# Performance work log

Measured on AMD Instinct MI355X. Metric: run time of the kernel, lower is better.

## Reference

```python
import jax, jax.numpy as jnp
import numpy as np

N = 100000
E = 1000000
N_FEAT = 128
N_HID = 16
N_HEAD = 8
HIDDEN = N_HID * N_HEAD  # 128
N_CLASS = 64
NEG_SLOPE = 0.2


def layer_norm(x, g, b, eps=1e-5):
    mu = x.mean(-1, keepdims=True)
    var = ((x - mu) ** 2).mean(-1, keepdims=True)
    return (x - mu) * jax.lax.rsqrt(var + eps) * g + b


def gat_conv(x, src, dst, W, a_src, a_dst, bias, concat):
    # Standard GATConv math (PyG): project, per-head additive attention,
    # softmax over incoming edges (self-loops included), weighted scatter-sum.
    H, C = a_src.shape
    n = x.shape[0]
    h = (x @ W).reshape(n, H, C)                      # [N,H,C]
    al = jnp.einsum('nhc,hc->nh', h, a_src)           # [N,H]
    ar = jnp.einsum('nhc,hc->nh', h, a_dst)
    e = jax.nn.leaky_relu(al[src] + ar[dst], NEG_SLOPE)  # [E',H]
    m = jax.ops.segment_max(e, dst, num_segments=n)
    m = jnp.where(jnp.isfinite(m), m, 0.0)
    ee = jnp.exp(e - m[dst])
    den = jax.ops.segment_sum(ee, dst, num_segments=n)
    alpha = ee / (den[dst] + 1e-16)                   # [E',H]
    out = jax.ops.segment_sum(h[src] * alpha[:, :, None], dst, num_segments=n)
    out = out.reshape(n, H * C) if concat else out.mean(1)
    return out + bias, h, alpha


def setup_inputs() -> dict:
    key = jax.random.key(0)
    ks = jax.random.split(key, 20)
    s = lambda *sh: 1.0 / np.sqrt(sh[-1])
    inp = {
        'x': jax.random.normal(ks[0], (N, N_FEAT), jnp.float32),
        'edge_index': jax.random.randint(ks[1], (2, E), 0, N, jnp.int32),
        # layer 1: n_feat -> n_hid x n_head (concat)
        'W1': jax.random.normal(ks[2], (N_FEAT, HIDDEN), jnp.float32) * s(N_FEAT),
        'a_src1': jax.random.normal(ks[3], (N_HEAD, N_HID), jnp.float32) * s(N_HID),
        'a_dst1': jax.random.normal(ks[4], (N_HEAD, N_HID), jnp.float32) * s(N_HID),
        'b1': jnp.zeros((HIDDEN,), jnp.float32),
        'g1': jnp.ones((HIDDEN,), jnp.float32),
        'be1': jnp.zeros((HIDDEN,), jnp.float32),
        # layer 2: hidden -> hidden (concat)
        'W2': jax.random.normal(ks[5], (HIDDEN, HIDDEN), jnp.float32) * s(HIDDEN),
        'a_src2': jax.random.normal(ks[6], (N_HEAD, N_HID), jnp.float32) * s(N_HID),
        'a_dst2': jax.random.normal(ks[7], (N_HEAD, N_HID), jnp.float32) * s(N_HID),
        'b2': jnp.zeros((HIDDEN,), jnp.float32),
        'g2': jnp.ones((HIDDEN,), jnp.float32),
        'be2': jnp.zeros((HIDDEN,), jnp.float32),
        # out layer: hidden -> n_class, 1 head, concat=False
        'W3': jax.random.normal(ks[8], (HIDDEN, N_CLASS), jnp.float32) * s(HIDDEN),
        'a_src3': jax.random.normal(ks[9], (1, N_CLASS), jnp.float32) * s(N_CLASS),
        'a_dst3': jax.random.normal(ks[10], (1, N_CLASS), jnp.float32) * s(N_CLASS),
        'b3': jnp.zeros((N_CLASS,), jnp.float32),
        'g3': jnp.ones((N_CLASS,), jnp.float32),
        'be3': jnp.zeros((N_CLASS,), jnp.float32),
    }
    return inp


def reference(x, edge_index, W1, a_src1, a_dst1, b1, g1, be1,
              W2, a_src2, a_dst2, b2, g2, be2,
              W3, a_src3, a_dst3, b3, g3, be3):
    # add self loops (GATConv default)
    loops = jnp.arange(N, dtype=edge_index.dtype)
    src = jnp.concatenate([edge_index[0], loops])
    dst = jnp.concatenate([edge_index[1], loops])
    # Transductive path, eval mode (dropout is identity)
    x, _, _ = gat_conv(x, src, dst, W1, a_src1, a_dst1, b1, concat=True)
    x = jax.nn.elu(layer_norm(x, g1, be1))
    x, _, _ = gat_conv(x, src, dst, W2, a_src2, a_dst2, b2, concat=True)
    x = jax.nn.elu(layer_norm(x, g2, be2))
    x, _, _ = gat_conv(x, src, dst, W3, a_src3, a_dst3, b3, concat=False)
    x = layer_norm(x, g3, be3)
    return x
```

## Files before the change

kernel.cpp:

```cpp
#include <hip/hip_runtime.h>
#include <math.h>

#define N_NODES 100000
#define N_EDGES 1000000
#define EP_EDGES (N_EDGES + N_NODES)
#define NBKT ((N_NODES + 255) / 256)

typedef short bf16x8 __attribute__((ext_vector_type(8)));
typedef float f32x4 __attribute__((ext_vector_type(4)));


__device__ inline unsigned bf16pack(float a, float b) {
    unsigned ua = __float_as_uint(a);
    unsigned ub = __float_as_uint(b);
    ua += 0x7FFFu + ((ua >> 16) & 1u);
    ub += 0x7FFFu + ((ub >> 16) & 1u);
    return (ua >> 16) | (ub & 0xFFFF0000u);
}

__device__ inline unsigned short bf16r(float a) {
    unsigned u = __float_as_uint(a);
    u += 0x7FFFu + ((u >> 16) & 1u);
    return (unsigned short)(u >> 16);
}

__device__ inline int swz(int o) { return o ^ (((o >> 8) & 7) << 4); }


__global__ void bkt_count(const int* __restrict__ ei, int* __restrict__ bktCnt) {
    __shared__ int hist[NBKT];
    int tid = threadIdx.x;
    for (int j = tid; j < NBKT; j += 256) hist[j] = 0;
    __syncthreads();
    int e0 = blockIdx.x * 4096;
    int e1 = min(e0 + 4096, EP_EDGES);
    for (int e = e0 + tid; e < e1; e += 256) {
        int d = (e < N_EDGES) ? ei[N_EDGES + e] : (e - N_EDGES);
        atomicAdd(&hist[d >> 8], 1);
    }
    __syncthreads();
    for (int j = tid; j < NBKT; j += 256) {
        int c = hist[j];
        if (c) atomicAdd(&bktCnt[j], c);
    }
}

__global__ void bkt_scan(const int* __restrict__ bktCnt, int* __restrict__ bktBase,
                         int* __restrict__ bktCursor, int* __restrict__ rs) {
    __shared__ int tmp[512];
    int tid = threadIdx.x;
    int v = (tid < NBKT) ? bktCnt[tid] : 0;
    tmp[tid] = v;
    __syncthreads();
    int run = v;
    for (int off = 1; off < 512; off <<= 1) {
        int add = (tid >= off) ? tmp[tid - off] : 0;
        __syncthreads();
        run += add;
        tmp[tid] = run;
        __syncthreads();
    }
    if (tid <= NBKT) {
        int base = run - v;
        bktBase[tid] = base;
        if (tid < NBKT) bktCursor[tid] = base;
    }
    if (tid == 0) rs[N_NODES] = EP_EDGES;
}

__global__ void bkt_scatter(const int* __restrict__ ei, int* __restrict__ bktCursor,
                            unsigned* __restrict__ bktEdges) {
    __shared__ int hist[NBKT], chunk[NBKT];
    int tid = threadIdx.x;
    for (int j = tid; j < NBKT; j += 256) hist[j] = 0;
    __syncthreads();
    int e0 = blockIdx.x * 2048;
    int e1 = min(e0 + 2048, EP_EDGES);
    for (int e = e0 + tid; e < e1; e += 256) {
        int d = (e < N_EDGES) ? ei[N_EDGES + e] : (e - N_EDGES);
        atomicAdd(&hist[d >> 8], 1);
    }
    __syncthreads();
    for (int j = tid; j < NBKT; j += 256) {
        int c = hist[j];
        chunk[j] = c ? atomicAdd(&bktCursor[j], c) : 0;
        hist[j] = 0;
    }
    __syncthreads();
    for (int e = e0 + tid; e < e1; e += 256) {
        int s, d;
        if (e < N_EDGES) { s = ei[e]; d = ei[N_EDGES + e]; }
        else             { s = d = e - N_EDGES; }
        int b = d >> 8;
        int off = atomicAdd(&hist[b], 1);
        bktEdges[chunk[b] + off] = (unsigned)s | ((unsigned)(d & 255) << 24);
    }
}

__global__ void bkt_final(const unsigned* __restrict__ bktEdges, const int* __restrict__ bktBase,
                          int* __restrict__ rs, int* __restrict__ csr_src) {
    __shared__ int hist[256], excl[256], tmp[256], cur[256];
    int tid = threadIdx.x;
    int b = blockIdx.x;
    int base = bktBase[b], end = bktBase[b + 1];
    hist[tid] = 0;
    __syncthreads();
    for (int i = base + tid; i < end; i += 256)
        atomicAdd(&hist[bktEdges[i] >> 24], 1);
    __syncthreads();
    int v = hist[tid];
    tmp[tid] = v;
    __syncthreads();
    int run = v;
    for (int off = 1; off < 256; off <<= 1) {
        int add = (tid >= off) ? tmp[tid - off] : 0;
        __syncthreads();
        run += add;
        tmp[tid] = run;
        __syncthreads();
    }
    excl[tid] = run - v;
    cur[tid] = 0;
    int node = b * 256 + tid;
    if (node < N_NODES) rs[node] = base + excl[tid];
    __syncthreads();
    for (int i = base + tid; i < end; i += 256) {
        unsigned u = bktEdges[i];
        int d = u >> 24;
        int pos = base + excl[d] + atomicAdd(&cur[d], 1);
        csr_src[pos] = (int)(u & 0xFFFFFFu);
    }
}


template <int COUT>
__global__ void wt_prep(const float* __restrict__ W, unsigned short* __restrict__ Wt) {
    int t = blockIdx.x * 256 + threadIdx.x;
    if (t >= 128 * COUT) return;
    int k = t / COUT, c = t % COUT;
    Wt[c * 128 + k] = bf16r(W[t]);
}


template <int COUT, int H, bool IN_F32>
__launch_bounds__(256)
__global__ void gemm_mfma(const void* __restrict__ Xv, const unsigned short* __restrict__ Wt,
                          const float* __restrict__ a_src, const float* __restrict__ a_dst,
                          unsigned* __restrict__ hb16, float* __restrict__ al,
                          float* __restrict__ ar, int n) {
    constexpr int NT = COUT / 16;
    __shared__ unsigned char lds[16384 + COUT * 256 + 1024];
    unsigned char* sx = lds;
    unsigned char* sw = lds + 16384;
    float* sc = (float*)sw;

    int tid = threadIdx.x;
    int row0 = blockIdx.x * 64;
    int lane = tid & 63;
    int wv = tid >> 6;

    if (IN_F32) {
        const float* Xf = (const float*)Xv;
        for (int c = tid; c < 1024; c += 256) {
            int o = c * 16;
            int row = o >> 8;
            int k0 = (o & 255) >> 1;
            int gr = row0 + row;
            float4 f0 = make_float4(0.f, 0.f, 0.f, 0.f), f1 = f0;
            if (gr < n) {
                f0 = *(const float4*)(Xf + (size_t)gr * 128 + k0);
                f1 = *(const float4*)(Xf + (size_t)gr * 128 + k0 + 4);
            }
            *(uint4*)(sx + swz(o)) = make_uint4(bf16pack(f0.x, f0.y), bf16pack(f0.z, f0.w),
                                                bf16pack(f1.x, f1.y), bf16pack(f1.z, f1.w));
        }
    } else {
        const unsigned char* Xb = (const unsigned char*)Xv;
        for (int c = tid; c < 1024; c += 256) {
            int o = c * 16;
            int row = o >> 8;
            int gr = row0 + row;
            uint4 v = make_uint4(0u, 0u, 0u, 0u);
            if (gr < n) v = *(const uint4*)(Xb + (size_t)gr * 256 + (o & 255));
            *(uint4*)(sx + swz(o)) = v;
        }
    }
    for (int c = tid; c < COUT * 16; c += 256) {
        int o = c * 16;
        *(uint4*)(sw + swz(o)) = *(const uint4*)((const unsigned char*)Wt + o);
    }
    __syncthreads();

    f32x4 acc[NT];
#pragma unroll
    for (int t = 0; t < NT; ++t) acc[t] = (f32x4){0.f, 0.f, 0.f, 0.f};
    int arow = wv * 16 + (lane & 15);
    int kg = lane >> 4;
#pragma unroll
    for (int s = 0; s < 4; ++s) {
        int ko = s * 64 + kg * 16;
        bf16x8 a = *(const bf16x8*)(sx + swz(arow * 256 + ko));
#pragma unroll
        for (int t = 0; t < NT; ++t) {
            bf16x8 bfr = *(const bf16x8*)(sw + swz((t * 16 + (lane & 15)) * 256 + ko));
            acc[t] = __builtin_amdgcn_mfma_f32_16x16x32_bf16(a, bfr, acc[t], 0, 0, 0);
        }
    }
    __syncthreads();

#pragma unroll
    for (int t = 0; t < NT; ++t)
#pragma unroll
        for (int i = 0; i < 4; ++i)
            sc[(wv * 16 + kg * 4 + i) * (COUT + 4) + t * 16 + (lane & 15)] = acc[t][i];
    __syncthreads();

    constexpr int NCG = COUT / 8;
    constexpr int ROWS = 64 * NCG / 256;
    int tc = tid % NCG, tr = tid / NCG;
    float asv[8], adv[8];
#pragma unroll
    for (int j = 0; j < 8; ++j) {
        asv[j] = a_src[tc * 8 + j];
        adv[j] = a_dst[tc * 8 + j];
    }
#pragma unroll
    for (int i = 0; i < ROWS; ++i) {
        int row = tr * ROWS + i;
        int gr = row0 + row;
        float h8[8];
        *(float4*)&h8[0] = *(const float4*)(sc + row * (COUT + 4) + tc * 8);
        *(float4*)&h8[4] = *(const float4*)(sc + row * (COUT + 4) + tc * 8 + 4);
        float pa = 0.f, pb = 0.f;
#pragma unroll
        for (int j = 0; j < 8; ++j) {
            pa = fmaf(h8[j], asv[j], pa);
            pb = fmaf(h8[j], adv[j], pb);
        }
        if (COUT / H == 16) {
            pa += __shfl_xor(pa, 1);
            pb += __shfl_xor(pb, 1);
            if ((tc & 1) == 0 && gr < n) {
                al[gr * H + (tc >> 1)] = pa;
                ar[gr * H + (tc >> 1)] = pb;
            }
        } else {
            pa += __shfl_xor(pa, 1); pb += __shfl_xor(pb, 1);
            pa += __shfl_xor(pa, 2); pb += __shfl_xor(pb, 2);
            pa += __shfl_xor(pa, 4); pb += __shfl_xor(pb, 4);
            if (tc == 0 && gr < n) {
                al[gr] = pa;
                ar[gr] = pb;
            }
        }
        if (gr < n) {
            *(uint4*)(hb16 + (size_t)gr * (COUT / 2) + tc * 4) =
                make_uint4(bf16pack(h8[0], h8[1]), bf16pack(h8[2], h8[3]),
                           bf16pack(h8[4], h8[5]), bf16pack(h8[6], h8[7]));
        }
    }
}


template <int H, int COUT, bool DO_ELU, bool OUTBF>
__launch_bounds__(256)
__global__ void gat_fused(const unsigned* __restrict__ hb16, const float* __restrict__ al,
                          const float* __restrict__ ar, const int* __restrict__ row_start,
                          const int* __restrict__ csr_src, const float* __restrict__ bias,
                          const float* __restrict__ gamma, const float* __restrict__ beta,
                          void* __restrict__ outx, int n) {
    constexpr bool PAIR = (COUT == 128);
    constexpr int C = COUT / H;
    int node = blockIdx.x * 4 + (threadIdx.x >> 6);
    node = __builtin_amdgcn_readfirstlane(node);
    int l = threadIdx.x & 63;
    if (node >= n) return;

    int c0 = PAIR ? 2 * l : l;
    int hc = c0 / C;
    float arh = ar[node * H + hc];

    int rsv = row_start[node];
    int deg = row_start[node + 1] - rsv;
    const int* sp = csr_src + rsv;
    const unsigned short* hbs = (const unsigned short*)hb16;

    float acc0 = 0.f, acc1 = 0.f, den = 0.f;

    int k = 0;
    for (; k + 4 <= deg; k += 4) {
        int s0 = sp[k + 0], s1 = sp[k + 1], s2 = sp[k + 2], s3 = sp[k + 3];
        float a0 = al[s0 * H + hc], a1 = al[s1 * H + hc];
        float a2 = al[s2 * H + hc], a3 = al[s3 * H + hc];
        float e0 = a0 + arh; e0 = (e0 >= 0.f) ? e0 : 0.2f * e0;
        float e1 = a1 + arh; e1 = (e1 >= 0.f) ? e1 : 0.2f * e1;
        float e2 = a2 + arh; e2 = (e2 >= 0.f) ? e2 : 0.2f * e2;
        float e3 = a3 + arh; e3 = (e3 >= 0.f) ? e3 : 0.2f * e3;
        float w0 = __expf(e0), w1 = __expf(e1), w2 = __expf(e2), w3 = __expf(e3);
        den += (w0 + w1) + (w2 + w3);
        if (PAIR) {
            unsigned u0 = hb16[(size_t)s0 * 64 + l];
            unsigned u1 = hb16[(size_t)s1 * 64 + l];
            unsigned u2 = hb16[(size_t)s2 * 64 + l];
            unsigned u3 = hb16[(size_t)s3 * 64 + l];
            acc0 = fmaf(w0, __uint_as_float(u0 << 16), acc0);
            acc1 = fmaf(w0, __uint_as_float(u0 & 0xFFFF0000u), acc1);
            acc0 = fmaf(w1, __uint_as_float(u1 << 16), acc0);
            acc1 = fmaf(w1, __uint_as_float(u1 & 0xFFFF0000u), acc1);
            acc0 = fmaf(w2, __uint_as_float(u2 << 16), acc0);
            acc1 = fmaf(w2, __uint_as_float(u2 & 0xFFFF0000u), acc1);
            acc0 = fmaf(w3, __uint_as_float(u3 << 16), acc0);
            acc1 = fmaf(w3, __uint_as_float(u3 & 0xFFFF0000u), acc1);
        } else {
            float r0 = __uint_as_float(((unsigned)hbs[(size_t)s0 * 64 + l]) << 16);
            float r1 = __uint_as_float(((unsigned)hbs[(size_t)s1 * 64 + l]) << 16);
            float r2 = __uint_as_float(((unsigned)hbs[(size_t)s2 * 64 + l]) << 16);
            float r3 = __uint_as_float(((unsigned)hbs[(size_t)s3 * 64 + l]) << 16);
            acc0 = fmaf(w0, r0, acc0);
            acc0 = fmaf(w1, r1, acc0);
            acc0 = fmaf(w2, r2, acc0);
            acc0 = fmaf(w3, r3, acc0);
        }
    }
    for (; k < deg; ++k) {
        int s0 = sp[k];
        float a0 = al[s0 * H + hc];
        float e0 = a0 + arh; e0 = (e0 >= 0.f) ? e0 : 0.2f * e0;
        float w0 = __expf(e0);
        den += w0;
        if (PAIR) {
            unsigned u0 = hb16[(size_t)s0 * 64 + l];
            acc0 = fmaf(w0, __uint_as_float(u0 << 16), acc0);
            acc1 = fmaf(w0, __uint_as_float(u0 & 0xFFFF0000u), acc1);
        } else {
            float r0 = __uint_as_float(((unsigned)hbs[(size_t)s0 * 64 + l]) << 16);
            acc0 = fmaf(w0, r0, acc0);
        }
    }

    float inv = 1.f / (den + 1e-16f);
    float v0 = acc0 * inv + bias[c0];
    float v1 = 0.f;
    float ssum = v0;
    if (PAIR) { v1 = acc1 * inv + bias[c0 + 1]; ssum += v1; }
    for (int off = 1; off < 64; off <<= 1) ssum += __shfl_xor(ssum, off);
    float mean = ssum / COUT;
    float d0 = v0 - mean, d1 = v1 - mean;
    float vs = PAIR ? (d0 * d0 + d1 * d1) : d0 * d0;
    for (int off = 1; off < 64; off <<= 1) vs += __shfl_xor(vs, off);
    float rstd = rsqrtf(vs / COUT + 1e-5f);
    float y0 = d0 * rstd * gamma[c0] + beta[c0];
    if (DO_ELU) y0 = (y0 > 0.f) ? y0 : expm1f(y0);
    if (PAIR) {
        float y1 = d1 * rstd * gamma[c0 + 1] + beta[c0 + 1];
        if (DO_ELU) y1 = (y1 > 0.f) ? y1 : expm1f(y1);
        if (OUTBF) {
            ((unsigned*)outx)[(size_t)node * 64 + l] = bf16pack(y0, y1);
        } else {
            *(float2*)((float*)outx + (size_t)node * COUT + c0) = make_float2(y0, y1);
        }
    } else {
        ((float*)outx)[(size_t)node * COUT + c0] = y0;
    }
}


extern "C" void kernel_launch(void* const* d_in, const int* in_sizes, int n_in,
                              void* d_out, int out_size, void* d_ws, size_t ws_size,
                              hipStream_t stream) {
    const float* x   = (const float*)d_in[0];
    const int*   ei  = (const int*)d_in[1];
    const float* W1  = (const float*)d_in[2];
    const float* as1 = (const float*)d_in[3];
    const float* ad1 = (const float*)d_in[4];
    const float* b1  = (const float*)d_in[5];
    const float* g1  = (const float*)d_in[6];
    const float* be1 = (const float*)d_in[7];
    const float* W2  = (const float*)d_in[8];
    const float* as2 = (const float*)d_in[9];
    const float* ad2 = (const float*)d_in[10];
    const float* b2  = (const float*)d_in[11];
    const float* g2  = (const float*)d_in[12];
    const float* be2 = (const float*)d_in[13];
    const float* W3  = (const float*)d_in[14];
    const float* as3 = (const float*)d_in[15];
    const float* ad3 = (const float*)d_in[16];
    const float* b3  = (const float*)d_in[17];
    const float* g3  = (const float*)d_in[18];
    const float* be3 = (const float*)d_in[19];
    float* out = (float*)d_out;

    char* p = (char*)d_ws;
    auto alloc = [&](size_t bytes) -> char* {
        char* r = p;
        p += (bytes + 255) & ~size_t(255);
        return r;
    };
    unsigned* hb16   = (unsigned*)alloc((size_t)N_NODES * 64 * 4);
    unsigned* xbuf   = (unsigned*)alloc((size_t)N_NODES * 64 * 4);
    float* al        = (float*)alloc((size_t)N_NODES * 8 * 4);
    float* ar        = (float*)alloc((size_t)N_NODES * 8 * 4);
    int*   rs        = (int*)alloc((size_t)(N_NODES + 1) * 4);
    int*   csr_src   = (int*)alloc((size_t)EP_EDGES * 4);
    unsigned* bktEdges = (unsigned*)alloc((size_t)EP_EDGES * 4);
    int*   bktCnt    = (int*)alloc((size_t)(NBKT + 1) * 4);
    int*   bktBase   = (int*)alloc((size_t)(NBKT + 1) * 4);
    int*   bktCursor = (int*)alloc((size_t)(NBKT + 1) * 4);
    unsigned short* Wt1 = (unsigned short*)alloc((size_t)128 * 128 * 2);
    unsigned short* Wt2 = (unsigned short*)alloc((size_t)128 * 128 * 2);
    unsigned short* Wt3 = (unsigned short*)alloc((size_t)64 * 128 * 2);

    hipMemsetAsync(bktCnt, 0, (size_t)(NBKT + 1) * 4, stream);

    wt_prep<128><<<64, 256, 0, stream>>>(W1, Wt1);
    wt_prep<128><<<64, 256, 0, stream>>>(W2, Wt2);
    wt_prep<64><<<32, 256, 0, stream>>>(W3, Wt3);

    bkt_count<<<(EP_EDGES + 4095) / 4096, 256, 0, stream>>>(ei, bktCnt);
    bkt_scan<<<1, 512, 0, stream>>>(bktCnt, bktBase, bktCursor, rs);
    bkt_scatter<<<(EP_EDGES + 2047) / 2048, 256, 0, stream>>>(ei, bktCursor, bktEdges);
    bkt_final<<<NBKT, 256, 0, stream>>>(bktEdges, bktBase, rs, csr_src);

    const int gemm_grid = (N_NODES + 63) / 64;
    const int agg_grid  = (N_NODES + 3) / 4;

    gemm_mfma<128, 8, true><<<gemm_grid, 256, 0, stream>>>(x, Wt1, as1, ad1,
                                                           hb16, al, ar, N_NODES);
    gat_fused<8, 128, true, true><<<agg_grid, 256, 0, stream>>>(hb16, al, ar, rs, csr_src,
                                                                b1, g1, be1, xbuf, N_NODES);
    gemm_mfma<128, 8, false><<<gemm_grid, 256, 0, stream>>>(xbuf, Wt2, as2, ad2,
                                                            hb16, al, ar, N_NODES);
    gat_fused<8, 128, true, true><<<agg_grid, 256, 0, stream>>>(hb16, al, ar, rs, csr_src,
                                                                b2, g2, be2, xbuf, N_NODES);
    gemm_mfma<64, 1, false><<<gemm_grid, 256, 0, stream>>>(xbuf, Wt3, as3, ad3,
                                                           hb16, al, ar, N_NODES);
    gat_fused<1, 64, false, false><<<agg_grid, 256, 0, stream>>>(hb16, al, ar, rs, csr_src,
                                                                 b3, g3, be3, out, N_NODES);
}
```

Measured before the change: 294.3 us.

## Compute attention weights edge-parallel across lanes and broadcast them for gathers

The aggregation loop now spreads the edge-index loads and the exp of the attention logits across lanes, with each lane covering one (edge, head) pair. Before, every lane recomputed the weights for four edges at a time. Source ids and weights are broadcast with readlane/shfl, and the next batch of source indices is prefetched. The denominator is reduced through a cross-lane shuffle. This removes redundant exp and scalar-index loads, at the cost of extra shuffles and masked padding work when node degree is low (mean about 11).

```diff
diff --git a/kernel.cpp b/kernel.cpp
--- a/kernel.cpp
+++ b/kernel.cpp
@@ -270,73 +270,78 @@
                           const float* __restrict__ gamma, const float* __restrict__ beta,
                           void* __restrict__ outx, int n) {
     constexpr bool PAIR = (COUT == 128);
-    constexpr int C = COUT / H;
+    constexpr int LOGH = (H == 8) ? 3 : 0;
+    constexpr int G = 64 >> LOGH;
     int node = blockIdx.x * 4 + (threadIdx.x >> 6);
     node = __builtin_amdgcn_readfirstlane(node);
     int l = threadIdx.x & 63;
     if (node >= n) return;
 
     int c0 = PAIR ? 2 * l : l;
-    int hc = c0 / C;
-    float arh = ar[node * H + hc];
+    int hc = c0 / (COUT / H);
+    int eh = l & (H - 1);
+    int ej = l >> LOGH;
+    float ar_e = ar[node * H + eh];
 
     int rsv = row_start[node];
     int deg = row_start[node + 1] - rsv;
     const int* sp = csr_src + rsv;
     const unsigned short* hbs = (const unsigned short*)hb16;
 
-    float acc0 = 0.f, acc1 = 0.f, den = 0.f;
-
-    int k = 0;
-    for (; k + 4 <= deg; k += 4) {
-        int s0 = sp[k + 0], s1 = sp[k + 1], s2 = sp[k + 2], s3 = sp[k + 3];
-        float a0 = al[s0 * H + hc], a1 = al[s1 * H + hc];
-        float a2 = al[s2 * H + hc], a3 = al[s3 * H + hc];
-        float e0 = a0 + arh; e0 = (e0 >= 0.f) ? e0 : 0.2f * e0;
-        float e1 = a1 + arh; e1 = (e1 >= 0.f) ? e1 : 0.2f * e1;
-        float e2 = a2 + arh; e2 = (e2 >= 0.f) ? e2 : 0.2f * e2;
-        float e3 = a3 + arh; e3 = (e3 >= 0.f) ? e3 : 0.2f * e3;
-        float w0 = __expf(e0), w1 = __expf(e1), w2 = __expf(e2), w3 = __expf(e3);
-        den += (w0 + w1) + (w2 + w3);
+    float acc0 = 0.f, acc1 = 0.f, den_p = 0.f;
+
+    int i0 = ej < deg ? ej : deg - 1;
+    int s_cur = sp[i0];
+
+    for (int k = 0; k < deg; k += G) {
+        int s_nxt = s_cur;
+        if (k + G < deg) {
+            int idn = k + G + ej;
+            idn = idn < deg ? idn : deg - 1;
+            s_nxt = sp[idn];
+        }
+        float a = al[s_cur * H + eh];
+        float e = a + ar_e;
+        e = (e >= 0.f) ? e : 0.2f * e;
+        float w = ((k + ej) < deg) ? __expf(e) : 0.f;
+        den_p += w;
+
         if (PAIR) {
-            unsigned u0 = hb16[(size_t)s0 * 64 + l];
-            unsigned u1 = hb16[(size_t)s1 * 64 + l];
-            unsigned u2 = hb16[(size_t)s2 * 64 + l];
-            unsigned u3 = hb16[(size_t)s3 * 64 + l];
-            acc0 = fmaf(w0, __uint_as_float(u0 << 16), acc0);
-            acc1 = fmaf(w0, __uint_as_float(u0 & 0xFFFF0000u), acc1);
-            acc0 = fmaf(w1, __uint_as_float(u1 << 16), acc0);
-            acc1 = fmaf(w1, __uint_as_float(u1 & 0xFFFF0000u), acc1);
-            acc0 = fmaf(w2, __uint_as_float(u2 << 16), acc0);
-            acc1 = fmaf(w2, __uint_as_float(u2 & 0xFFFF0000u), acc1);
-            acc0 = fmaf(w3, __uint_as_float(u3 << 16), acc0);
-            acc1 = fmaf(w3, __uint_as_float(u3 & 0xFFFF0000u), acc1);
+            unsigned rv[8];
+#pragma unroll
+            for (int j = 0; j < 8; ++j) {
+                int sj = __builtin_amdgcn_readlane(s_cur, j * 8);
+                rv[j] = *(hb16 + (size_t)sj * 64 + l);
+            }
+#pragma unroll
+            for (int j = 0; j < 8; ++j) {
+                float wj = __shfl(w, j * 8 + hc);
+                acc0 = fmaf(wj, __uint_as_float(rv[j] << 16), acc0);
+                acc1 = fmaf(wj, __uint_as_float(rv[j] & 0xFFFF0000u), acc1);
+            }
         } else {
-            float r0 = __uint_as_float(((unsigned)hbs[(size_t)s0 * 64 + l]) << 16);
-            float r1 = __uint_as_float(((unsigned)hbs[(size_t)s1 * 64 + l]) << 16);
-            float r2 = __uint_as_float(((unsigned)hbs[(size_t)s2 * 64 + l]) << 16);
-            float r3 = __uint_as_float(((unsigned)hbs[(size_t)s3 * 64 + l]) << 16);
-            acc0 = fmaf(w0, r0, acc0);
-            acc0 = fmaf(w1, r1, acc0);
-            acc0 = fmaf(w2, r2, acc0);
-            acc0 = fmaf(w3, r3, acc0);
-        }
-    }
-    for (; k < deg; ++k) {
-        int s0 = sp[k];
-        float a0 = al[s0 * H + hc];
-        float e0 = a0 + arh; e0 = (e0 >= 0.f) ? e0 : 0.2f * e0;
-        float w0 = __expf(e0);
-        den += w0;
-        if (PAIR) {
-            unsigned u0 = hb16[(size_t)s0 * 64 + l];
-            acc0 = fmaf(w0, __uint_as_float(u0 << 16), acc0);
-            acc1 = fmaf(w0, __uint_as_float(u0 & 0xFFFF0000u), acc1);
-        } else {
-            float r0 = __uint_as_float(((unsigned)hbs[(size_t)s0 * 64 + l]) << 16);
-            acc0 = fmaf(w0, r0, acc0);
-        }
-    }
+#pragma unroll
+            for (int sub = 0; sub < 8; ++sub) {
+                if (k + sub * 8 >= deg) break;
+                unsigned short rv[8];
+#pragma unroll
+                for (int j2 = 0; j2 < 8; ++j2) {
+                    int sj = __builtin_amdgcn_readlane(s_cur, sub * 8 + j2);
+                    rv[j2] = hbs[(size_t)sj * 64 + l];
+                }
+#pragma unroll
+                for (int j2 = 0; j2 < 8; ++j2) {
+                    float wj = __uint_as_float(
+                        __builtin_amdgcn_readlane(__float_as_uint(w), sub * 8 + j2));
+                    acc0 = fmaf(wj, __uint_as_float(((unsigned)rv[j2]) << 16), acc0);
+                }
+            }
+        }
+        s_cur = s_nxt;
+    }
+
+    for (int off = H; off < 64; off <<= 1) den_p += __shfl_xor(den_p, off);
+    float den = __shfl(den_p, hc);
 
     float inv = 1.f / (den + 1e-16f);
     float v0 = acc0 * inv + bias[c0];
```

Measured after the change: 284.7 us. 1.03x faster.
